# Optimization experiments

Hardware: AMD Instinct MI355X
Metric: run time of the kernel (lower is better)

Reference implementation:

```python
import jax, jax.numpy as jnp
import numpy as np

D_MODEL = 1024
N_HEADS = 16
N_KV = 4
HEAD_DIM = 64
R = 256
B, N = 2, 2048


def setup_inputs() -> dict:
    key = jax.random.key(0)
    ks = jax.random.split(key, 5)
    x = jax.random.normal(ks[0], (B, N, D_MODEL), jnp.float32)
    # rotary cos/sin table: (N, HEAD_DIM//2, 2)
    inv = 1.0 / (10000.0 ** (jnp.arange(0, HEAD_DIM, 2, dtype=jnp.float32) / HEAD_DIM))
    ang = jnp.arange(N, dtype=jnp.float32)[:, None] * inv[None, :]
    freqs_cis = jnp.stack([jnp.cos(ang), jnp.sin(ang)], axis=-1)
    s = 0.02
    Wq = jax.random.normal(ks[1], (D_MODEL, N_HEADS * HEAD_DIM), jnp.float32) * s
    Wk = jax.random.normal(ks[2], (D_MODEL, N_KV * HEAD_DIM), jnp.float32) * s
    Wv = jax.random.normal(ks[3], (D_MODEL, N_KV * HEAD_DIM), jnp.float32) * s
    Wo = jax.random.normal(ks[4], (N_HEADS * HEAD_DIM, D_MODEL), jnp.float32) * s
    return dict(x=x, freqs_cis=freqs_cis, Wq=Wq, Wk=Wk, Wv=Wv, Wo=Wo)


def _select_pairs(scores_i, best_b_i, r):
    """Greedy top-r pair selection with unique-b constraint (one batch row)."""
    half = scores_i.shape[0]
    order = jnp.argsort(-scores_i)  # descending by best similarity

    def step(carry, a_local):
        used, count = carry
        b_local = best_b_i[a_local]
        take = jnp.logical_and(jnp.logical_not(used[b_local]), count < r)
        used = used.at[b_local].set(used[b_local] | take)
        count = count + take.astype(jnp.int32)
        return (used, count), (take, a_local.astype(jnp.int32), b_local.astype(jnp.int32))

    (_, count), (takes, a_locs, b_locs) = jax.lax.scan(
        step, (jnp.zeros(half, bool), jnp.int32(0)), order)
    pos = jnp.cumsum(takes.astype(jnp.int32)) - 1
    idx = jnp.where(takes, pos, r)  # dump non-taken into slot r
    sel_a = jnp.zeros(r + 1, jnp.int32).at[idx].set(a_locs)[:r]
    sel_b = jnp.zeros(r + 1, jnp.int32).at[idx].set(b_locs)[:r]
    valid = jnp.arange(r) < count  # pad (if fewer than r unique) with first pair
    sel_a = jnp.where(valid, sel_a, sel_a[0])
    sel_b = jnp.where(valid, sel_b, sel_b[0])
    return sel_a, sel_b


def bipartite_indices(metric, r):
    """Returns (global_a, global_b, keep_idx) for merge/unmerge."""
    Bm, Nm, _ = metric.shape
    a = metric[:, 0::2]  # (B, half, C)
    b = metric[:, 1::2]
    an = a / jnp.maximum(jnp.linalg.norm(a, axis=-1, keepdims=True), 1e-12)
    bn = b / jnp.maximum(jnp.linalg.norm(b, axis=-1, keepdims=True), 1e-12)
    scores = jnp.einsum('bic,bjc->bij', an, bn)  # (B, half, half)
    best_scores = scores.max(axis=2)
    best_b = scores.argmax(axis=2)
    sel_a, sel_b = jax.vmap(lambda s, m: _select_pairs(s, m, r))(best_scores, best_b)
    global_a = 2 * sel_a      # even indices
    global_b = 2 * sel_b + 1  # odd indices
    bidx = jnp.arange(Bm)[:, None]
    keep_mask = jnp.ones((Bm, Nm), bool).at[bidx, global_b].set(False)
    # stable argsort puts kept (False) positions first, in original order
    keep_idx = jnp.argsort(~keep_mask, axis=1)[:, :Nm - r]
    return global_a, global_b, keep_idx


def merge(x, global_a, global_b, keep_idx):
    Bm = x.shape[0]
    bidx = jnp.arange(Bm)[:, None]
    xa = jnp.take_along_axis(x, global_a[..., None], axis=1)
    xb = jnp.take_along_axis(x, global_b[..., None], axis=1)
    x_out = x.at[bidx, global_a].set((xa + xb) * 0.5)
    return jnp.take_along_axis(x_out, keep_idx[..., None], axis=1)


def unmerge(xm, global_a, global_b, keep_idx, n_orig):
    Bm, _, C = xm.shape
    bidx = jnp.arange(Bm)[:, None]
    out = jnp.zeros((Bm, n_orig, C), xm.dtype).at[bidx, keep_idx].set(xm)
    xa = jnp.take_along_axis(out, global_a[..., None], axis=1)
    return out.at[bidx, global_b].set(xa)


def _rope(t, freqs):
    # t: (B, N, H, HD), freqs: (N, HD//2, 2)
    cos = freqs[None, :, None, :, 0]
    sin = freqs[None, :, None, :, 1]
    t1 = t[..., 0::2]
    t2 = t[..., 1::2]
    rot = jnp.stack([t1 * cos - t2 * sin, t1 * sin + t2 * cos], axis=-1)
    return rot.reshape(t.shape)


def _attention(x_m, freqs, Wq, Wk, Wv, Wo):
    Bm, Nm, _ = x_m.shape
    q = (x_m @ Wq).reshape(Bm, Nm, N_HEADS, HEAD_DIM)
    k = (x_m @ Wk).reshape(Bm, Nm, N_KV, HEAD_DIM)
    v = (x_m @ Wv).reshape(Bm, Nm, N_KV, HEAD_DIM)
    q = _rope(q, freqs)
    k = _rope(k, freqs)
    rep = N_HEADS // N_KV
    k = jnp.repeat(k, rep, axis=2)
    v = jnp.repeat(v, rep, axis=2)
    att = jnp.einsum('bqhd,bkhd->bhqk', q, k) / np.sqrt(HEAD_DIM).astype(np.float32)
    w = jax.nn.softmax(att, axis=-1)
    o = jnp.einsum('bhqk,bkhd->bqhd', w, v).reshape(Bm, Nm, N_HEADS * HEAD_DIM)
    return o @ Wo


def reference(x, freqs_cis, Wq, Wk, Wv, Wo):
    n = x.shape[1]
    metric = jax.lax.stop_gradient(x @ Wk)  # k_proj under no_grad
    ga, gb, ki = bipartite_indices(metric, R)
    x_m = merge(x, ga, gb, ki)
    n_merged = x_m.shape[1]
    out_m = _attention(x_m, freqs_cis[:n_merged], Wq, Wk, Wv, Wo)
    return unmerge(out_m, ga, gb, ki, n)
```

## Files before the change

### kernel.cpp

```cpp
#include <hip/hip_runtime.h>
#include <hip/hip_bf16.h>
#include <math.h>

#define BB 2
#define NN 2048
#define DM 1024
#define NH 16
#define NKV 4
#define HD 64
#define RR 256
#define HALF 1024
#define NM 1792
#define NT 28
#define NSPL 4

typedef __bf16 bf16x8 __attribute__((ext_vector_type(8)));
typedef float f32x4 __attribute__((ext_vector_type(4)));

__device__ inline unsigned pk2(float a, float b) {
  union { __bf16 h; unsigned short u; } ua, ub;
  ua.h = (__bf16)a;
  ub.h = (__bf16)b;
  return (unsigned)ua.u | ((unsigned)ub.u << 16);
}

__device__ inline unsigned shu(unsigned v, int s) {
  return (unsigned)__shfl((int)v, s, 64);
}

__device__ __forceinline__ void async16(const void* g, void* l) {
  __builtin_amdgcn_global_load_lds(
      (const __attribute__((address_space(1))) void*)g,
      (__attribute__((address_space(3))) void*)l, 16, 0, 0);
}

__global__ __launch_bounds__(256) void gemm_bf16(
    const __bf16* __restrict__ A, const __bf16* __restrict__ Bt,
    float* __restrict__ C, int M, int N, int K) {
  __shared__ __align__(16) __bf16 As[8192];
  __shared__ __align__(16) __bf16 Bs[4096];
  const int bm0 = blockIdx.x * 128;
  const int bn0 = blockIdx.y * 64;
  const int w = threadIdx.x >> 6;
  const int lane = threadIdx.x & 63;
  f32x4 acc[2][4];
#pragma unroll
  for (int i = 0; i < 2; ++i)
#pragma unroll
    for (int nt = 0; nt < 4; ++nt) acc[i][nt] = (f32x4){0.f, 0.f, 0.f, 0.f};
  for (int kk = 0; kk < K; kk += 64) {
    __syncthreads();
#pragma unroll
    for (int it = 0; it < 4; ++it) {
      const int c = it * 256 + w * 64 + lane;
      async16(A + (size_t)(bm0 + ((c >> 7) << 4) + (c & 15)) * K + kk +
                  (((c >> 6) & 1) << 5) + (((c >> 4) & 3) << 3),
              &As[(it * 256 + w * 64) * 8]);
    }
#pragma unroll
    for (int it = 0; it < 2; ++it) {
      const int c = it * 256 + w * 64 + lane;
      async16(Bt + (size_t)(bn0 + ((c >> 7) << 4) + (c & 15)) * K + kk +
                  (((c >> 6) & 1) << 5) + (((c >> 4) & 3) << 3),
              &Bs[(it * 256 + w * 64) * 8]);
    }
    __syncthreads();
#pragma unroll
    for (int s = 0; s < 2; ++s) {
      bf16x8 a0 = *(const bf16x8*)&As[((2 * w) * 128 + s * 64 + lane) * 8];
      bf16x8 a1 = *(const bf16x8*)&As[((2 * w + 1) * 128 + s * 64 + lane) * 8];
#pragma unroll
      for (int nt = 0; nt < 4; ++nt) {
        bf16x8 bfr = *(const bf16x8*)&Bs[(nt * 128 + s * 64 + lane) * 8];
        acc[0][nt] =
            __builtin_amdgcn_mfma_f32_16x16x32_bf16(a0, bfr, acc[0][nt], 0, 0, 0);
        acc[1][nt] =
            __builtin_amdgcn_mfma_f32_16x16x32_bf16(a1, bfr, acc[1][nt], 0, 0, 0);
      }
    }
  }
  const int g = lane >> 4, ml = lane & 15;
#pragma unroll
  for (int i = 0; i < 2; ++i)
#pragma unroll
    for (int nt = 0; nt < 4; ++nt)
#pragma unroll
      for (int r = 0; r < 4; ++r)
        C[(size_t)(bm0 + (2 * w + i) * 16 + g * 4 + r) * N + bn0 + nt * 16 +
          ml] = acc[i][nt][r];
}

__global__ __launch_bounds__(256) void gemm_wo(
    const __bf16* __restrict__ A, const __bf16* __restrict__ Bt,
    const int* __restrict__ keep_idx, const int* __restrict__ dst2,
    float* __restrict__ out, int M, int N, int K) {
  __shared__ __align__(16) __bf16 As[8192];
  __shared__ __align__(16) __bf16 Bs[4096];
  const int bm0 = blockIdx.x * 128;
  const int bn0 = blockIdx.y * 64;
  const int w = threadIdx.x >> 6;
  const int lane = threadIdx.x & 63;
  f32x4 acc[2][4];
#pragma unroll
  for (int i = 0; i < 2; ++i)
#pragma unroll
    for (int nt = 0; nt < 4; ++nt) acc[i][nt] = (f32x4){0.f, 0.f, 0.f, 0.f};
  for (int kk = 0; kk < K; kk += 64) {
    __syncthreads();
#pragma unroll
    for (int it = 0; it < 4; ++it) {
      const int c = it * 256 + w * 64 + lane;
      async16(A + (size_t)(bm0 + ((c >> 7) << 4) + (c & 15)) * K + kk +
                  (((c >> 6) & 1) << 5) + (((c >> 4) & 3) << 3),
              &As[(it * 256 + w * 64) * 8]);
    }
#pragma unroll
    for (int it = 0; it < 2; ++it) {
      const int c = it * 256 + w * 64 + lane;
      async16(Bt + (size_t)(bn0 + ((c >> 7) << 4) + (c & 15)) * K + kk +
                  (((c >> 6) & 1) << 5) + (((c >> 4) & 3) << 3),
              &Bs[(it * 256 + w * 64) * 8]);
    }
    __syncthreads();
#pragma unroll
    for (int s = 0; s < 2; ++s) {
      bf16x8 a0 = *(const bf16x8*)&As[((2 * w) * 128 + s * 64 + lane) * 8];
      bf16x8 a1 = *(const bf16x8*)&As[((2 * w + 1) * 128 + s * 64 + lane) * 8];
#pragma unroll
      for (int nt = 0; nt < 4; ++nt) {
        bf16x8 bfr = *(const bf16x8*)&Bs[(nt * 128 + s * 64 + lane) * 8];
        acc[0][nt] =
            __builtin_amdgcn_mfma_f32_16x16x32_bf16(a0, bfr, acc[0][nt], 0, 0, 0);
        acc[1][nt] =
            __builtin_amdgcn_mfma_f32_16x16x32_bf16(a1, bfr, acc[1][nt], 0, 0, 0);
      }
    }
  }
  const int g = lane >> 4, ml = lane & 15;
#pragma unroll
  for (int i = 0; i < 2; ++i)
#pragma unroll
    for (int r = 0; r < 4; ++r) {
      const int row = bm0 + (2 * w + i) * 16 + g * 4 + r;
      const int bb = row / NM, tt = row % NM;
      const int p1 = keep_idx[bb * NM + tt];
      const int p2 = dst2[bb * NM + tt];
#pragma unroll
      for (int nt = 0; nt < 4; ++nt) {
        const int col = bn0 + nt * 16 + ml;
        float v = acc[i][nt][r];
        out[((size_t)(bb * NN + p1)) * DM + col] = v;
        if (p2 >= 0) out[((size_t)(bb * NN + p2)) * DM + col] = v;
      }
    }
}

__global__ __launch_bounds__(256) void gemm3t(
    const __bf16* __restrict__ Ah, const __bf16* __restrict__ Al,
    const __bf16* __restrict__ Bh, const __bf16* __restrict__ Bl,
    float* __restrict__ C0, float* __restrict__ C1, int M, int N, int K) {
  __shared__ __align__(16) __bf16 Ahs[4096], Als[4096], Bhs[4096], Bls[4096];
  const int z = blockIdx.z;
  float* C = z ? C1 : C0;
  const int kof = z * (K / 2);
  const int bm0 = blockIdx.x * 64;
  const int bn0 = blockIdx.y * 64;
  const int w = threadIdx.x >> 6;
  const int lane = threadIdx.x & 63;
  f32x4 acc[4];
#pragma unroll
  for (int nt = 0; nt < 4; ++nt) acc[nt] = (f32x4){0.f, 0.f, 0.f, 0.f};
  for (int kk = kof; kk < kof + K / 2; kk += 64) {
    __syncthreads();
#pragma unroll
    for (int it = 0; it < 2; ++it) {
      const int c = it * 256 + w * 64 + lane;
      const size_t ra = (size_t)(bm0 + ((c >> 7) << 4) + (c & 15)) * K;
      const size_t rb = (size_t)(bn0 + ((c >> 7) << 4) + (c & 15)) * K;
      const int col = kk + (((c >> 6) & 1) << 5) + (((c >> 4) & 3) << 3);
      const int lb = (it * 256 + w * 64) * 8;
      async16(Ah + ra + col, &Ahs[lb]);
      async16(Al + ra + col, &Als[lb]);
      async16(Bh + rb + col, &Bhs[lb]);
      async16(Bl + rb + col, &Bls[lb]);
    }
    __syncthreads();
#pragma unroll
    for (int s = 0; s < 2; ++s) {
      bf16x8 ah = *(const bf16x8*)&Ahs[((w * 2 + s) * 64 + lane) * 8];
      bf16x8 al = *(const bf16x8*)&Als[((w * 2 + s) * 64 + lane) * 8];
#pragma unroll
      for (int nt = 0; nt < 4; ++nt) {
        bf16x8 bh = *(const bf16x8*)&Bhs[((nt * 2 + s) * 64 + lane) * 8];
        bf16x8 bl = *(const bf16x8*)&Bls[((nt * 2 + s) * 64 + lane) * 8];
        acc[nt] = __builtin_amdgcn_mfma_f32_16x16x32_bf16(al, bh, acc[nt], 0, 0, 0);
        acc[nt] = __builtin_amdgcn_mfma_f32_16x16x32_bf16(ah, bl, acc[nt], 0, 0, 0);
        acc[nt] = __builtin_amdgcn_mfma_f32_16x16x32_bf16(ah, bh, acc[nt], 0, 0, 0);
      }
    }
  }
  const int g = lane >> 4, ml = lane & 15;
#pragma unroll
  for (int nt = 0; nt < 4; ++nt)
#pragma unroll
    for (int r = 0; r < 4; ++r)
      C[(size_t)(bm0 + w * 16 + g * 4 + r) * N + bn0 + nt * 16 + ml] =
          acc[nt][r];
}

__global__ __launch_bounds__(256) void gemm_scam(
    const __bf16* __restrict__ Ah, const __bf16* __restrict__ Al,
    const __bf16* __restrict__ Bh, const __bf16* __restrict__ Bl,
    float* __restrict__ sval, int* __restrict__ sidx) {
  __shared__ __align__(16) __bf16 Ahs[4096], Als[4096], Bhs[4096], Bls[4096];
  const size_t zo = (size_t)blockIdx.z * HALF * 256;
  const int bm0 = blockIdx.x * 64;
  const int bn0 = blockIdx.y * 64;
  const int w = threadIdx.x >> 6;
  const int lane = threadIdx.x & 63;
  f32x4 acc[4];
#pragma unroll
  for (int nt = 0; nt < 4; ++nt) acc[nt] = (f32x4){0.f, 0.f, 0.f, 0.f};
  for (int kk = 0; kk < 256; kk += 64) {
    __syncthreads();
#pragma unroll
    for (int it = 0; it < 2; ++it) {
      const int c = it * 256 + w * 64 + lane;
      const size_t ra = zo + (size_t)(bm0 + ((c >> 7) << 4) + (c & 15)) * 256;
      const size_t rb = zo + (size_t)(bn0 + ((c >> 7) << 4) + (c & 15)) * 256;
      const int col = kk + (((c >> 6) & 1) << 5) + (((c >> 4) & 3) << 3);
      const int lb = (it * 256 + w * 64) * 8;
      async16(Ah + ra + col, &Ahs[lb]);
      async16(Al + ra + col, &Als[lb]);
      async16(Bh + rb + col, &Bhs[lb]);
      async16(Bl + rb + col, &Bls[lb]);
    }
    __syncthreads();
#pragma unroll
    for (int s = 0; s < 2; ++s) {
      bf16x8 ah = *(const bf16x8*)&Ahs[((w * 2 + s) * 64 + lane) * 8];
      bf16x8 al = *(const bf16x8*)&Als[((w * 2 + s) * 64 + lane) * 8];
#pragma unroll
      for (int nt = 0; nt < 4; ++nt) {
        bf16x8 bh = *(const bf16x8*)&Bhs[((nt * 2 + s) * 64 + lane) * 8];
        bf16x8 bl = *(const bf16x8*)&Bls[((nt * 2 + s) * 64 + lane) * 8];
        acc[nt] = __builtin_amdgcn_mfma_f32_16x16x32_bf16(al, bh, acc[nt], 0, 0, 0);
        acc[nt] = __builtin_amdgcn_mfma_f32_16x16x32_bf16(ah, bl, acc[nt], 0, 0, 0);
        acc[nt] = __builtin_amdgcn_mfma_f32_16x16x32_bf16(ah, bh, acc[nt], 0, 0, 0);
      }
    }
  }
  const int g = lane >> 4, ml = lane & 15;
#pragma unroll
  for (int r = 0; r < 4; ++r) {
    float bv = acc[0][r];
    int bc = bn0 + ml;
#pragma unroll
    for (int nt = 1; nt < 4; ++nt) {
      float v = acc[nt][r];
      int c = bn0 + nt * 16 + ml;
      if (v > bv) { bv = v; bc = c; }
    }
#pragma unroll
    for (int off = 1; off < 16; off <<= 1) {
      float vo = __shfl_xor(bv, off, 64);
      int co = __shfl_xor(bc, off, 64);
      if (vo > bv || (vo == bv && co < bc)) { bv = vo; bc = co; }
    }
    if (ml == 0) {
      const int row = bm0 + w * 16 + g * 4 + r;
      const size_t o = ((size_t)blockIdx.z * HALF + row) * 16 + (bn0 >> 6);
      sval[o] = bv;
      sidx[o] = bc;
    }
  }
}

__global__ __launch_bounds__(256) void argmax_reduce(
    const float* __restrict__ sval, const int* __restrict__ sidx,
    float* __restrict__ best_s, int* __restrict__ best_b) {
  const int lane = threadIdx.x & 63;
  const int e = lane & 15;
  const int rid = blockIdx.x * 16 + (threadIdx.x >> 6) * 4 + (lane >> 4);
  float bv = sval[rid * 16 + e];
  int bc = sidx[rid * 16 + e];
#pragma unroll
  for (int off = 1; off < 16; off <<= 1) {
    float vo = __shfl_xor(bv, off, 64);
    int co = __shfl_xor(bc, off, 64);
    if (vo > bv || (vo == bv && co < bc)) { bv = vo; bc = co; }
  }
  if (e == 0) {
    best_s[rid] = bv;
    best_b[rid] = bc;
  }
}

__global__ __launch_bounds__(256) void hilo_split(const float* __restrict__ x,
                                                  __bf16* __restrict__ xh,
                                                  __bf16* __restrict__ xl) {
  const int i = blockIdx.x * 256 + threadIdx.x;
  float4 v = ((const float4*)x)[i];
  float f[4] = {v.x, v.y, v.z, v.w};
  union { __bf16 h[4]; uint2 u; } H, L;
#pragma unroll
  for (int j = 0; j < 4; ++j) {
    __bf16 hh = (__bf16)f[j];
    H.h[j] = hh;
    L.h[j] = (__bf16)(f[j] - (float)hh);
  }
  ((uint2*)xh)[i] = H.u;
  ((uint2*)xl)[i] = L.u;
}

__global__ __launch_bounds__(256) void transpose_all(
    const float* __restrict__ Wq, const float* __restrict__ Wk,
    const float* __restrict__ Wv, const float* __restrict__ Wo,
    __bf16* __restrict__ Wqkvt, __bf16* __restrict__ Wktl,
    __bf16* __restrict__ Wot) {
  __shared__ float ld[64][65];
  const int z = blockIdx.x;
  const float* src;
  __bf16* dsth;
  __bf16* dstl = nullptr;
  int N, k0, n0, rowoff;
  if (z < 256) {
    src = Wq; N = 1024; k0 = (z >> 4) << 6; n0 = (z & 15) << 6;
    dsth = Wqkvt; rowoff = 0;
  } else if (z < 320) {
    int zz = z - 256;
    src = Wk; N = 256; k0 = (zz >> 2) << 6; n0 = (zz & 3) << 6;
    dsth = Wqkvt; rowoff = 1024; dstl = Wktl;
  } else if (z < 384) {
    int zz = z - 320;
    src = Wv; N = 256; k0 = (zz >> 2) << 6; n0 = (zz & 3) << 6;
    dsth = Wqkvt; rowoff = 1280;
  } else {
    int zz = z - 384;
    src = Wo; N = 1024; k0 = (zz >> 4) << 6; n0 = (zz & 15) << 6;
    dsth = Wot; rowoff = 0;
  }
  for (int i = threadIdx.x; i < 1024; i += 256) {
    int r = i >> 4, c4 = i & 15;
    float4 v = *(const float4*)(src + (size_t)(k0 + r) * N + n0 + c4 * 4);
    ld[r][c4 * 4 + 0] = v.x;
    ld[r][c4 * 4 + 1] = v.y;
    ld[r][c4 * 4 + 2] = v.z;
    ld[r][c4 * 4 + 3] = v.w;
  }
  __syncthreads();
  for (int i = threadIdx.x; i < 4096; i += 256) {
    int n = i >> 6, k = i & 63;
    float v = ld[k][n];
    __bf16 hh = (__bf16)v;
    dsth[(size_t)(rowoff + n0 + n) * 1024 + k0 + k] = hh;
    if (dstl)
      dstl[(size_t)(n0 + n) * 1024 + k0 + k] = (__bf16)(v - (float)hh);
  }
}

__global__ __launch_bounds__(256) void normalize_split(
    const float* __restrict__ m0, const float* __restrict__ m1,
    __bf16* __restrict__ anh, __bf16* __restrict__ anl,
    __bf16* __restrict__ bnh, __bf16* __restrict__ bnl) {
  const int row = blockIdx.x;
  const int b = row >> 11;
  const int r = row & 2047;
  const int t = threadIdx.x;
  float v = m0[(size_t)row * 256 + t] + m1[(size_t)row * 256 + t];
  float ss = v * v;
#pragma unroll
  for (int o = 32; o > 0; o >>= 1) ss += __shfl_xor(ss, o, 64);
  __shared__ float wsum[4];
  if ((t & 63) == 0) wsum[t >> 6] = ss;
  __syncthreads();
  float tot = wsum[0] + wsum[1] + wsum[2] + wsum[3];
  float inv = 1.f / fmaxf(sqrtf(tot), 1e-12f);
  float nv = v * inv;
  __bf16 hh = (__bf16)nv;
  __bf16 ll = (__bf16)(nv - (float)hh);
  size_t o = ((size_t)b * HALF + (r >> 1)) * 256 + t;
  if (r & 1) {
    bnh[o] = hh;
    bnl[o] = ll;
  } else {
    anh[o] = hh;
    anl[o] = ll;
  }
}

__global__ __launch_bounds__(512) void sort_desc(const float* __restrict__ best_s,
                                                 int* __restrict__ order) {
  const int b = blockIdx.x;
  __shared__ float sv[1024];
  __shared__ int si[1024];
  for (int i = threadIdx.x; i < 1024; i += 512) {
    sv[i] = best_s[b * HALF + i];
    si[i] = i;
  }
  __syncthreads();
  for (int k = 2; k <= 1024; k <<= 1) {
    for (int j = k >> 1; j > 0; j >>= 1) {
      for (int t = threadIdx.x; t < 1024; t += 512) {
        int ixj = t ^ j;
        if (ixj > t) {
          bool dir = ((t & k) == 0);
          float va = sv[t], vb = sv[ixj];
          int ia = si[t], ib = si[ixj];
          bool before = (vb > va) || (vb == va && ib < ia);
          if (before == dir) {
            sv[t] = vb; sv[ixj] = va;
            si[t] = ib; si[ixj] = ia;
          }
        }
      }
      __syncthreads();
    }
  }
  for (int i = threadIdx.x; i < 1024; i += 512) order[b * HALF + i] = si[i];
}

__global__ __launch_bounds__(256) void select_and_index(
    const int* __restrict__ best_b, const int* __restrict__ order,
    int* __restrict__ keep_idx, int* __restrict__ partner,
    int* __restrict__ dst2) {
  const int b = blockIdx.x;
  __shared__ int rankA[HALF];
  __shared__ int minrank[HALF];
  __shared__ int taken[HALF];
  __shared__ int sel_a[RR], sel_b[RR];
  __shared__ int removed[NN];
  __shared__ int src_row[NN];
  __shared__ int tsum[256];
  const int t = threadIdx.x;

  for (int i = t; i < HALF; i += 256) { minrank[i] = 0x7fffffff; taken[i] = 0; }
  for (int i = t; i < NN; i += 256) {
    removed[i] = 0;
    partner[b * NN + i] = -1;
  }
  for (int i = t; i < NM; i += 256) dst2[b * NM + i] = -1;
  __syncthreads();
  int ord[4];
#pragma unroll
  for (int q = 0; q < 4; ++q) {
    int step = t * 4 + q;
    ord[q] = order[b * HALF + step];
    rankA[ord[q]] = step;
  }
  __syncthreads();
#pragma unroll
  for (int q = 0; q < 4; ++q) {
    int a = t * 4 + q;
    atomicMin(&minrank[best_b[b * HALF + a]], rankA[a]);
  }
  __syncthreads();
  for (int i = t; i < HALF; i += 256) {
    int mr = minrank[i];
    if (mr != 0x7fffffff) taken[mr] = 1;
  }
  __syncthreads();
  int c[4];
  int mysum = 0;
#pragma unroll
  for (int q = 0; q < 4; ++q) { c[q] = taken[t * 4 + q]; mysum += c[q]; }
  tsum[t] = mysum;
  __syncthreads();
  for (int off = 1; off < 256; off <<= 1) {
    int v = (t >= off) ? tsum[t - off] : 0;
    __syncthreads();
    tsum[t] += v;
    __syncthreads();
  }
  int run = tsum[t] - mysum;
#pragma unroll
  for (int q = 0; q < 4; ++q) {
    if (c[q] && run < RR) {
      int a = ord[q];
      sel_a[run] = 2 * a;
      sel_b[run] = 2 * best_b[b * HALF + a] + 1;
    }
    run += c[q];
  }
  __syncthreads();
  const int cnt = min(tsum[255], RR);
  if (t >= cnt) { sel_a[t] = sel_a[0]; sel_b[t] = sel_b[0]; }
  __syncthreads();
  {
    int ga = sel_a[t], gb = sel_b[t];
    removed[gb] = 1;
    partner[b * NN + ga] = gb;
  }
  __syncthreads();
  int myc = 0;
#pragma unroll
  for (int q = 0; q < 8; ++q) myc += !removed[8 * t + q];
  tsum[t] = myc;
  __syncthreads();
  for (int off = 1; off < 256; off <<= 1) {
    int v = (t >= off) ? tsum[t - off] : 0;
    __syncthreads();
    tsum[t] += v;
    __syncthreads();
  }
  int pos = tsum[t] - myc;
#pragma unroll
  for (int q = 0; q < 8; ++q) {
    int p = 8 * t + q;
    int sr = -1;
    if (!removed[p]) {
      if (pos < NM) {
        keep_idx[b * NM + pos] = p;
        sr = pos;
      }
      ++pos;
    }
    src_row[p] = sr;
  }
  __syncthreads();
  {
    int sr = src_row[sel_a[t]];
    dst2[b * NM + sr] = sel_b[t];
  }
}

__global__ __launch_bounds__(256) void merge_kernel(
    const float* __restrict__ x, const int* __restrict__ keep_idx,
    const int* __restrict__ partner, __bf16* __restrict__ x_mb) {
  const int mrow = blockIdx.x;
  const int b = mrow / NM;
  const int t = mrow % NM;
  const int p = keep_idx[b * NM + t];
  const int pp = partner[b * NN + p];
  const float4* src =
      reinterpret_cast<const float4*>(x + ((size_t)b * NN + p) * DM);
  float4 val = src[threadIdx.x];
  if (pp >= 0) {
    const float4* s2 =
        reinterpret_cast<const float4*>(x + ((size_t)b * NN + pp) * DM);
    float4 v2 = s2[threadIdx.x];
    val.x = 0.5f * (val.x + v2.x);
    val.y = 0.5f * (val.y + v2.y);
    val.z = 0.5f * (val.z + v2.z);
    val.w = 0.5f * (val.w + v2.w);
  }
  union { __bf16 h[4]; uint2 u; } U;
  U.h[0] = (__bf16)val.x;
  U.h[1] = (__bf16)val.y;
  U.h[2] = (__bf16)val.z;
  U.h[3] = (__bf16)val.w;
  ((uint2*)(x_mb + (size_t)mrow * DM))[threadIdx.x] = U.u;
}

__global__ __launch_bounds__(256) void rope_fused(
    const float* __restrict__ qkv, const float* __restrict__ fc,
    __bf16* __restrict__ qbh, __bf16* __restrict__ kbh) {
  const int row = blockIdx.x;
  const int t = row % NM;
  const int b = row / NM;
  for (int idx = threadIdx.x; idx < 640; idx += 256) {
    int u = idx & 31;
    float c = fc[(t * 32 + u) * 2];
    float s = fc[(t * 32 + u) * 2 + 1];
    if (idx < 512) {
      int h = idx >> 5;
      const float* p = qkv + (size_t)row * 1536 + h * 64 + 2 * u;
      float x1 = p[0], x2 = p[1];
      __bf16* d = qbh + ((size_t)(b * NH + h) * NM + t) * 64 + 2 * u;
      d[0] = (__bf16)((x1 * c - x2 * s) * 0.125f);
      d[1] = (__bf16)((x1 * s + x2 * c) * 0.125f);
    } else {
      int h = (idx - 512) >> 5;
      const float* p = qkv + (size_t)row * 1536 + 1024 + h * 64 + 2 * u;
      float x1 = p[0], x2 = p[1];
      __bf16* d = kbh + ((size_t)(b * NKV + h) * NM + t) * 64 + 2 * u;
      d[0] = (__bf16)(x1 * c - x2 * s);
      d[1] = (__bf16)(x1 * s + x2 * c);
    }
  }
}

__global__ __launch_bounds__(256) void v_repack(const float* __restrict__ qkv,
                                                __bf16* __restrict__ vtb) {
  __shared__ float ld[64][65];
  int bid = blockIdx.x;
  const int kt = bid % (NM / 64); bid /= (NM / 64);
  const int kvh = bid % NKV;
  const int b = bid / NKV;
  const int j0 = kt * 64;
  for (int t2 = threadIdx.x; t2 < 1024; t2 += 256) {
    int key = t2 >> 4, c4 = t2 & 15;
    float4 v4 = *reinterpret_cast<const float4*>(
        qkv + (size_t)(b * NM + j0 + key) * 1536 + 1280 + kvh * 64 + c4 * 4);
    ld[key][c4 * 4 + 0] = v4.x;
    ld[key][c4 * 4 + 1] = v4.y;
    ld[key][c4 * 4 + 2] = v4.z;
    ld[key][c4 * 4 + 3] = v4.w;
  }
  __syncthreads();
  const int dim = threadIdx.x >> 2, kc = threadIdx.x & 3;
  __bf16* out = vtb + ((size_t)(b * NKV + kvh) * 64 + dim) * NM + j0 + kc * 16;
#pragma unroll
  for (int kk = 0; kk < 16; ++kk) out[kk] = (__bf16)ld[kc * 16 + kk][dim];
}

__global__ __launch_bounds__(512) void attn_mfma(
    const __bf16* __restrict__ qbh, const __bf16* __restrict__ kbh,
    const __bf16* __restrict__ vtb, float* __restrict__ pl,
    __bf16* __restrict__ pacc) {
  __shared__ __align__(16) __bf16 Ks[4096];
  __shared__ __align__(16) __bf16 Vs[4096];
  int bid = blockIdx.x;
  const int qt2 = bid % (NM / 32); bid /= (NM / 32);
  const int split = bid % NSPL; bid /= NSPL;
  const int kvh = bid % NKV;
  const int b = bid / NKV;
  const int w = threadIdx.x >> 6;
  const int lane = threadIdx.x & 63;
  const int h = kvh * 4 + (w & 3);
  const int qt = qt2 * 32 + (w >> 2) * 16;
  const int g = lane >> 4;
  const int ml = lane & 15;

  const __bf16* qrow = qbh + ((size_t)(b * NH + h) * NM + qt + ml) * 64;
  bf16x8 qa0 = *reinterpret_cast<const bf16x8*>(qrow + g * 8);
  bf16x8 qa1 = *reinterpret_cast<const bf16x8*>(qrow + 32 + g * 8);

  f32x4 acc[4];
#pragma unroll
  for (int mt = 0; mt < 4; ++mt) acc[mt] = (f32x4){0.f, 0.f, 0.f, 0.f};
  float lsum = 0.f;

  const __bf16* kp = kbh + (size_t)(b * NKV + kvh) * NM * 64;
  const __bf16* vp = vtb + (size_t)(b * NKV + kvh) * 64 * NM;
  const int src0 = ((lane >> 4) & 1) * 32 + ml;
  const int src1 = src0 + 16;
  const int sel = g >> 1;

  const int jt0 = split * (NT / NSPL);
  for (int jt = jt0; jt < jt0 + NT / NSPL; ++jt) {
    __syncthreads();
    {
      const int c = threadIdx.x;
      const int lb = (w * 64) * 8;
      async16(kp + (size_t)(jt * 64 + ((c >> 7) << 4) + (c & 15)) * 64 +
                  (((c >> 6) & 1) << 5) + (((c >> 4) & 3) << 3),
              &Ks[lb]);
      async16(vp + (size_t)(((c >> 7) << 4) + (c & 15)) * NM + jt * 64 +
                  (((c >> 6) & 1) << 5) + (((c >> 4) & 3) << 3),
              &Vs[lb]);
    }
    __syncthreads();
    f32x4 S[4];
#pragma unroll
    for (int nt = 0; nt < 4; ++nt) {
      bf16x8 k0 = *(const bf16x8*)&Ks[(nt * 128 + lane) * 8];
      bf16x8 k1 = *(const bf16x8*)&Ks[(nt * 128 + 64 + lane) * 8];
      f32x4 s4 = (f32x4){0.f, 0.f, 0.f, 0.f};
      s4 = __builtin_amdgcn_mfma_f32_16x16x32_bf16(k0, qa0, s4, 0, 0, 0);
      s4 = __builtin_amdgcn_mfma_f32_16x16x32_bf16(k1, qa1, s4, 0, 0, 0);
      S[nt] = s4;
    }
    float p[4][4];
#pragma unroll
    for (int nt = 0; nt < 4; ++nt)
#pragma unroll
      for (int r = 0; r < 4; ++r) {
        p[nt][r] = __expf(S[nt][r]);
        lsum += p[nt][r];
      }
    unsigned pk[4][2];
#pragma unroll
    for (int nt = 0; nt < 4; ++nt) {
      pk[nt][0] = pk2(p[nt][0], p[nt][1]);
      pk[nt][1] = pk2(p[nt][2], p[nt][3]);
    }
    unsigned A00 = shu(pk[0][0], src0), A01 = shu(pk[0][1], src0);
    unsigned A10 = shu(pk[1][0], src0), A11 = shu(pk[1][1], src0);
    unsigned B00 = shu(pk[0][0], src1), B01 = shu(pk[0][1], src1);
    unsigned B10 = shu(pk[1][0], src1), B11 = shu(pk[1][1], src1);
    unsigned C00 = shu(pk[2][0], src0), C01 = shu(pk[2][1], src0);
    unsigned C10 = shu(pk[3][0], src0), C11 = shu(pk[3][1], src0);
    unsigned D00 = shu(pk[2][0], src1), D01 = shu(pk[2][1], src1);
    unsigned D10 = shu(pk[3][0], src1), D11 = shu(pk[3][1], src1);
    union { uint4 u; bf16x8 v; } P0, P1;
    P0.u.x = sel ? A10 : A00; P0.u.y = sel ? A11 : A01;
    P0.u.z = sel ? B10 : B00; P0.u.w = sel ? B11 : B01;
    P1.u.x = sel ? C10 : C00; P1.u.y = sel ? C11 : C01;
    P1.u.z = sel ? D10 : D00; P1.u.w = sel ? D11 : D01;
#pragma unroll
    for (int mt = 0; mt < 4; ++mt) {
      bf16x8 v0 = *(const bf16x8*)&Vs[(mt * 128 + lane) * 8];
      bf16x8 v1 = *(const bf16x8*)&Vs[(mt * 128 + 64 + lane) * 8];
      acc[mt] = __builtin_amdgcn_mfma_f32_16x16x32_bf16(v0, P0.v, acc[mt], 0, 0, 0);
      acc[mt] = __builtin_amdgcn_mfma_f32_16x16x32_bf16(v1, P1.v, acc[mt], 0, 0, 0);
    }
  }
  lsum += __shfl_xor(lsum, 16, 64);
  lsum += __shfl_xor(lsum, 32, 64);
  const size_t row = (size_t)(b * NH + h) * NM + qt + ml;
  if (g == 0) pl[row * NSPL + split] = lsum;
  __bf16* pa = pacc + (row * NSPL + split) * 64;
#pragma unroll
  for (int mt = 0; mt < 4; ++mt) {
    uint2 u;
    u.x = pk2(acc[mt][0], acc[mt][1]);
    u.y = pk2(acc[mt][2], acc[mt][3]);
    *reinterpret_cast<uint2*>(pa + mt * 16 + g * 4) = u;
  }
}

__global__ __launch_bounds__(256) void attn_combine(
    const float* __restrict__ pl, const __bf16* __restrict__ pacc,
    __bf16* __restrict__ attn_ob) {
  const size_t rid = (size_t)blockIdx.x * 4 + (threadIdx.x >> 6);
  const int d = threadIdx.x & 63;
  float num = 0.f, den = 0.f;
#pragma unroll
  for (int s = 0; s < NSPL; ++s) {
    num += (float)pacc[(rid * NSPL + s) * 64 + d];
    den += pl[rid * NSPL + s];
  }
  float o = num / den;
  const int q = (int)(rid % NM);
  const int h = (int)((rid / NM) % NH);
  const int b = (int)(rid / ((size_t)NM * NH));
  attn_ob[((size_t)(b * NM + q)) * DM + h * 64 + d] = (__bf16)o;
}

extern "C" void kernel_launch(void* const* d_in, const int* in_sizes, int n_in,
                              void* d_out, int out_size, void* d_ws,
                              size_t ws_size, hipStream_t stream) {
  const float* x = (const float*)d_in[0];
  const float* fc = (const float*)d_in[1];
  const float* Wq = (const float*)d_in[2];
  const float* Wk = (const float*)d_in[3];
  const float* Wv = (const float*)d_in[4];
  const float* Wo = (const float*)d_in[5];
  float* out = (float*)d_out;

  char* ws = (char*)d_ws;
  size_t off = 0;
  auto alloc = [&](size_t bytes) {
    void* p = ws + off;
    off += (bytes + 255) & ~(size_t)255;
    return p;
  };
  float* metric0 = (float*)alloc((size_t)BB * NN * 256 * 4);
  float* metric1 = (float*)alloc((size_t)BB * NN * 256 * 4);
  float* best_s = (float*)alloc((size_t)BB * HALF * 4);
  int* best_b = (int*)alloc((size_t)BB * HALF * 4);
  int* order = (int*)alloc((size_t)BB * HALF * 4);
  int* keep_idx = (int*)alloc((size_t)BB * NM * 4);
  int* partner = (int*)alloc((size_t)BB * NN * 4);
  int* dst2 = (int*)alloc((size_t)BB * NM * 4);
  float* sval = (float*)alloc((size_t)BB * HALF * 16 * 4);
  int* sidx = (int*)alloc((size_t)BB * HALF * 16 * 4);
  char* bigreg = (char*)alloc((size_t)30 * 1024 * 1024);
  __bf16* xh = (__bf16*)bigreg;
  __bf16* xl = (__bf16*)(bigreg + (size_t)8704 * 1024);
  __bf16* anh = (__bf16*)bigreg;
  __bf16* anl = (__bf16*)(bigreg + (size_t)1100 * 1024);
  __bf16* bnh = (__bf16*)(bigreg + (size_t)2200 * 1024);
  __bf16* bnl = (__bf16*)(bigreg + (size_t)3300 * 1024);
  float* qkv = (float*)bigreg;
  __bf16* pacc = (__bf16*)bigreg;
  __bf16* x_mb = (__bf16*)alloc((size_t)BB * NM * DM * 2);
  __bf16* qbh = (__bf16*)alloc((size_t)BB * NH * NM * 64 * 2);
  __bf16* kbh = (__bf16*)alloc((size_t)BB * NKV * NM * 64 * 2);
  __bf16* vtb = (__bf16*)alloc((size_t)BB * NKV * 64 * NM * 2);
  __bf16* attn_ob = (__bf16*)alloc((size_t)BB * NM * DM * 2);
  float* pl = (float*)alloc((size_t)BB * NH * NM * NSPL * 4);
  __bf16* Wqkvt = (__bf16*)alloc((size_t)1536 * DM * 2);
  __bf16* Wktl = (__bf16*)alloc((size_t)256 * DM * 2);
  __bf16* Wot = (__bf16*)alloc((size_t)DM * DM * 2);
  const __bf16* Wkth = Wqkvt + (size_t)1024 * 1024;

  transpose_all<<<640, 256, 0, stream>>>(Wq, Wk, Wv, Wo, Wqkvt, Wktl, Wot);
  hilo_split<<<(BB * NN * DM / 4) / 256, 256, 0, stream>>>(x, xh, xl);
  gemm3t<<<dim3(64, 4, 2), 256, 0, stream>>>(xh, xl, Wkth, Wktl, metric0,
                                             metric1, BB * NN, 256, DM);
  normalize_split<<<BB * NN, 256, 0, stream>>>(metric0, metric1, anh, anl, bnh,
                                               bnl);
  gemm_scam<<<dim3(16, 16, 2), 256, 0, stream>>>(anh, anl, bnh, bnl, sval,
                                                 sidx);
  argmax_reduce<<<(BB * HALF) / 16, 256, 0, stream>>>(sval, sidx, best_s,
                                                      best_b);
  sort_desc<<<BB, 512, 0, stream>>>(best_s, order);
  select_and_index<<<BB, 256, 0, stream>>>(best_b, order, keep_idx, partner,
                                           dst2);
  merge_kernel<<<BB * NM, 256, 0, stream>>>(x, keep_idx, partner, x_mb);
  gemm_bf16<<<dim3(28, 24), 256, 0, stream>>>(x_mb, Wqkvt, qkv, BB * NM, 1536,
                                              DM);
  rope_fused<<<BB * NM, 256, 0, stream>>>(qkv, fc, qbh, kbh);
  v_repack<<<BB * NKV * (NM / 64), 256, 0, stream>>>(qkv, vtb);
  attn_mfma<<<BB * NKV * NSPL * (NM / 32), 512, 0, stream>>>(qbh, kbh, vtb, pl,
                                                             pacc);
  attn_combine<<<(BB * NH * NM) / 4, 256, 0, stream>>>(pl, pacc, attn_ob);
  gemm_wo<<<dim3(28, 16), 256, 0, stream>>>(attn_ob, Wot, keep_idx, dst2, out,
                                            BB * NM, DM, DM);
}
```

Measured before the change: 283.6 us.

## Merge small prep kernels, fold argmax into sort, double-buffer attention K/V loads

After: 291.6 us. 1.03x slower.

```diff
diff --git a/kernel.cpp b/kernel.cpp
--- a/kernel.cpp
+++ b/kernel.cpp
@@ -276,50 +276,29 @@
   }
 }
 
-__global__ __launch_bounds__(256) void argmax_reduce(
-    const float* __restrict__ sval, const int* __restrict__ sidx,
-    float* __restrict__ best_s, int* __restrict__ best_b) {
-  const int lane = threadIdx.x & 63;
-  const int e = lane & 15;
-  const int rid = blockIdx.x * 16 + (threadIdx.x >> 6) * 4 + (lane >> 4);
-  float bv = sval[rid * 16 + e];
-  int bc = sidx[rid * 16 + e];
-#pragma unroll
-  for (int off = 1; off < 16; off <<= 1) {
-    float vo = __shfl_xor(bv, off, 64);
-    int co = __shfl_xor(bc, off, 64);
-    if (vo > bv || (vo == bv && co < bc)) { bv = vo; bc = co; }
-  }
-  if (e == 0) {
-    best_s[rid] = bv;
-    best_b[rid] = bc;
-  }
-}
-
-__global__ __launch_bounds__(256) void hilo_split(const float* __restrict__ x,
-                                                  __bf16* __restrict__ xh,
-                                                  __bf16* __restrict__ xl) {
-  const int i = blockIdx.x * 256 + threadIdx.x;
-  float4 v = ((const float4*)x)[i];
-  float f[4] = {v.x, v.y, v.z, v.w};
-  union { __bf16 h[4]; uint2 u; } H, L;
-#pragma unroll
-  for (int j = 0; j < 4; ++j) {
-    __bf16 hh = (__bf16)f[j];
-    H.h[j] = hh;
-    L.h[j] = (__bf16)(f[j] - (float)hh);
-  }
-  ((uint2*)xh)[i] = H.u;
-  ((uint2*)xl)[i] = L.u;
-}
-
-__global__ __launch_bounds__(256) void transpose_all(
+__global__ __launch_bounds__(256) void prep_in(
     const float* __restrict__ Wq, const float* __restrict__ Wk,
     const float* __restrict__ Wv, const float* __restrict__ Wo,
-    __bf16* __restrict__ Wqkvt, __bf16* __restrict__ Wktl,
-    __bf16* __restrict__ Wot) {
+    const float* __restrict__ x, __bf16* __restrict__ Wqkvt,
+    __bf16* __restrict__ Wktl, __bf16* __restrict__ Wot,
+    __bf16* __restrict__ xh, __bf16* __restrict__ xl) {
+  const int z = blockIdx.x;
+  if (z >= 640) {
+    const int i = (z - 640) * 256 + threadIdx.x;
+    float4 v = ((const float4*)x)[i];
+    float f[4] = {v.x, v.y, v.z, v.w};
+    union { __bf16 h[4]; uint2 u; } H, L;
+#pragma unroll
+    for (int j = 0; j < 4; ++j) {
+      __bf16 hh = (__bf16)f[j];
+      H.h[j] = hh;
+      L.h[j] = (__bf16)(f[j] - (float)hh);
+    }
+    ((uint2*)xh)[i] = H.u;
+    ((uint2*)xl)[i] = L.u;
+    return;
+  }
   __shared__ float ld[64][65];
-  const int z = blockIdx.x;
   const float* src;
   __bf16* dsth;
   __bf16* dstl = nullptr;
@@ -389,14 +368,25 @@
   }
 }
 
-__global__ __launch_bounds__(512) void sort_desc(const float* __restrict__ best_s,
-                                                 int* __restrict__ order) {
+__global__ __launch_bounds__(512) void sort_desc(
+    const float* __restrict__ sval, const int* __restrict__ sidx,
+    int* __restrict__ best_b, int* __restrict__ order) {
   const int b = blockIdx.x;
   __shared__ float sv[1024];
   __shared__ int si[1024];
   for (int i = threadIdx.x; i < 1024; i += 512) {
-    sv[i] = best_s[b * HALF + i];
+    const size_t base = ((size_t)b * HALF + i) * 16;
+    float bv = sval[base];
+    int bc = sidx[base];
+#pragma unroll
+    for (int e = 1; e < 16; ++e) {
+      float v = sval[base + e];
+      int c = sidx[base + e];
+      if (v > bv || (v == bv && c < bc)) { bv = v; bc = c; }
+    }
+    sv[i] = bv;
     si[i] = i;
+    best_b[b * HALF + i] = bc;
   }
   __syncthreads();
   for (int k = 2; k <= 1024; k <<= 1) {
@@ -552,38 +542,39 @@
   ((uint2*)(x_mb + (size_t)mrow * DM))[threadIdx.x] = U.u;
 }
 
-__global__ __launch_bounds__(256) void rope_fused(
+__global__ __launch_bounds__(256) void prep_qkv(
     const float* __restrict__ qkv, const float* __restrict__ fc,
-    __bf16* __restrict__ qbh, __bf16* __restrict__ kbh) {
-  const int row = blockIdx.x;
-  const int t = row % NM;
-  const int b = row / NM;
-  for (int idx = threadIdx.x; idx < 640; idx += 256) {
-    int u = idx & 31;
-    float c = fc[(t * 32 + u) * 2];
-    float s = fc[(t * 32 + u) * 2 + 1];
-    if (idx < 512) {
-      int h = idx >> 5;
-      const float* p = qkv + (size_t)row * 1536 + h * 64 + 2 * u;
-      float x1 = p[0], x2 = p[1];
-      __bf16* d = qbh + ((size_t)(b * NH + h) * NM + t) * 64 + 2 * u;
-      d[0] = (__bf16)((x1 * c - x2 * s) * 0.125f);
-      d[1] = (__bf16)((x1 * s + x2 * c) * 0.125f);
-    } else {
-      int h = (idx - 512) >> 5;
-      const float* p = qkv + (size_t)row * 1536 + 1024 + h * 64 + 2 * u;
-      float x1 = p[0], x2 = p[1];
-      __bf16* d = kbh + ((size_t)(b * NKV + h) * NM + t) * 64 + 2 * u;
-      d[0] = (__bf16)(x1 * c - x2 * s);
-      d[1] = (__bf16)(x1 * s + x2 * c);
-    }
-  }
-}
-
-__global__ __launch_bounds__(256) void v_repack(const float* __restrict__ qkv,
-                                                __bf16* __restrict__ vtb) {
+    __bf16* __restrict__ qbh, __bf16* __restrict__ kbh,
+    __bf16* __restrict__ vtb) {
   __shared__ float ld[64][65];
-  int bid = blockIdx.x;
+  const int z = blockIdx.x;
+  if (z < BB * NM) {
+    const int row = z;
+    const int t = row % NM;
+    const int b = row / NM;
+    for (int idx = threadIdx.x; idx < 640; idx += 256) {
+      int u = idx & 31;
+      float c = fc[(t * 32 + u) * 2];
+      float s = fc[(t * 32 + u) * 2 + 1];
+      if (idx < 512) {
+        int h = idx >> 5;
+        const float* p = qkv + (size_t)row * 1536 + h * 64 + 2 * u;
+        float x1 = p[0], x2 = p[1];
+        __bf16* d = qbh + ((size_t)(b * NH + h) * NM + t) * 64 + 2 * u;
+        d[0] = (__bf16)((x1 * c - x2 * s) * 0.125f);
+        d[1] = (__bf16)((x1 * s + x2 * c) * 0.125f);
+      } else {
+        int h = (idx - 512) >> 5;
+        const float* p = qkv + (size_t)row * 1536 + 1024 + h * 64 + 2 * u;
+        float x1 = p[0], x2 = p[1];
+        __bf16* d = kbh + ((size_t)(b * NKV + h) * NM + t) * 64 + 2 * u;
+        d[0] = (__bf16)(x1 * c - x2 * s);
+        d[1] = (__bf16)(x1 * s + x2 * c);
+      }
+    }
+    return;
+  }
+  int bid = z - BB * NM;
   const int kt = bid % (NM / 64); bid /= (NM / 64);
   const int kvh = bid % NKV;
   const int b = bid / NKV;
@@ -608,8 +599,8 @@
     const __bf16* __restrict__ qbh, const __bf16* __restrict__ kbh,
     const __bf16* __restrict__ vtb, float* __restrict__ pl,
     __bf16* __restrict__ pacc) {
-  __shared__ __align__(16) __bf16 Ks[4096];
-  __shared__ __align__(16) __bf16 Vs[4096];
+  __shared__ __align__(16) __bf16 Ks[2][4096];
+  __shared__ __align__(16) __bf16 Vs[2][4096];
   int bid = blockIdx.x;
   const int qt2 = bid % (NM / 32); bid /= (NM / 32);
   const int split = bid % NSPL; bid /= NSPL;
@@ -636,26 +627,32 @@
   const int src0 = ((lane >> 4) & 1) * 32 + ml;
   const int src1 = src0 + 16;
   const int sel = g >> 1;
+  const int c = threadIdx.x;
+  const int lb = w * 512;
+  const size_t koff = (size_t)(((c >> 7) << 4) + (c & 15)) * 64 +
+                      (((c >> 6) & 1) << 5) + (((c >> 4) & 3) << 3);
+  const size_t voff = (size_t)(((c >> 7) << 4) + (c & 15)) * NM +
+                      (((c >> 6) & 1) << 5) + (((c >> 4) & 3) << 3);
 
   const int jt0 = split * (NT / NSPL);
-  for (int jt = jt0; jt < jt0 + NT / NSPL; ++jt) {
-    __syncthreads();
-    {
-      const int c = threadIdx.x;
-      const int lb = (w * 64) * 8;
-      async16(kp + (size_t)(jt * 64 + ((c >> 7) << 4) + (c & 15)) * 64 +
-                  (((c >> 6) & 1) << 5) + (((c >> 4) & 3) << 3),
-              &Ks[lb]);
-      async16(vp + (size_t)(((c >> 7) << 4) + (c & 15)) * NM + jt * 64 +
-                  (((c >> 6) & 1) << 5) + (((c >> 4) & 3) << 3),
-              &Vs[lb]);
-    }
-    __syncthreads();
+  const int niter = NT / NSPL;
+  async16(kp + (size_t)jt0 * 64 * 64 + koff, &Ks[0][lb]);
+  async16(vp + jt0 * 64 + voff, &Vs[0][lb]);
+
+  for (int i = 0; i < niter; ++i) {
+    __syncthreads();
+    if (i + 1 < niter) {
+      const int jn = jt0 + i + 1;
+      async16(kp + (size_t)jn * 64 * 64 + koff, &Ks[(i + 1) & 1][lb]);
+      async16(vp + jn * 64 + voff, &Vs[(i + 1) & 1][lb]);
+    }
+    const __bf16* Kb = Ks[i & 1];
+    const __bf16* Vb = Vs[i & 1];
     f32x4 S[4];
 #pragma unroll
     for (int nt = 0; nt < 4; ++nt) {
-      bf16x8 k0 = *(const bf16x8*)&Ks[(nt * 128 + lane) * 8];
-      bf16x8 k1 = *(const bf16x8*)&Ks[(nt * 128 + 64 + lane) * 8];
+      bf16x8 k0 = *(const bf16x8*)&Kb[(nt * 128 + lane) * 8];
+      bf16x8 k1 = *(const bf16x8*)&Kb[(nt * 128 + 64 + lane) * 8];
       f32x4 s4 = (f32x4){0.f, 0.f, 0.f, 0.f};
       s4 = __builtin_amdgcn_mfma_f32_16x16x32_bf16(k0, qa0, s4, 0, 0, 0);
       s4 = __builtin_amdgcn_mfma_f32_16x16x32_bf16(k1, qa1, s4, 0, 0, 0);
@@ -690,8 +687,8 @@
     P1.u.z = sel ? D10 : D00; P1.u.w = sel ? D11 : D01;
 #pragma unroll
     for (int mt = 0; mt < 4; ++mt) {
-      bf16x8 v0 = *(const bf16x8*)&Vs[(mt * 128 + lane) * 8];
-      bf16x8 v1 = *(const bf16x8*)&Vs[(mt * 128 + 64 + lane) * 8];
+      bf16x8 v0 = *(const bf16x8*)&Vb[(mt * 128 + lane) * 8];
+      bf16x8 v1 = *(const bf16x8*)&Vb[(mt * 128 + 64 + lane) * 8];
       acc[mt] = __builtin_amdgcn_mfma_f32_16x16x32_bf16(v0, P0.v, acc[mt], 0, 0, 0);
       acc[mt] = __builtin_amdgcn_mfma_f32_16x16x32_bf16(v1, P1.v, acc[mt], 0, 0, 0);
     }
@@ -748,7 +745,6 @@
   };
   float* metric0 = (float*)alloc((size_t)BB * NN * 256 * 4);
   float* metric1 = (float*)alloc((size_t)BB * NN * 256 * 4);
-  float* best_s = (float*)alloc((size_t)BB * HALF * 4);
   int* best_b = (int*)alloc((size_t)BB * HALF * 4);
   int* order = (int*)alloc((size_t)BB * HALF * 4);
   int* keep_idx = (int*)alloc((size_t)BB * NM * 4);
@@ -776,24 +772,22 @@
   __bf16* Wot = (__bf16*)alloc((size_t)DM * DM * 2);
   const __bf16* Wkth = Wqkvt + (size_t)1024 * 1024;
 
-  transpose_all<<<640, 256, 0, stream>>>(Wq, Wk, Wv, Wo, Wqkvt, Wktl, Wot);
-  hilo_split<<<(BB * NN * DM / 4) / 256, 256, 0, stream>>>(x, xh, xl);
+  prep_in<<<640 + (BB * NN * DM / 4) / 256, 256, 0, stream>>>(
+      Wq, Wk, Wv, Wo, x, Wqkvt, Wktl, Wot, xh, xl);
   gemm3t<<<dim3(64, 4, 2), 256, 0, stream>>>(xh, xl, Wkth, Wktl, metric0,
                                              metric1, BB * NN, 256, DM);
   normalize_split<<<BB * NN, 256, 0, stream>>>(metric0, metric1, anh, anl, bnh,
                                                bnl);
   gemm_scam<<<dim3(16, 16, 2), 256, 0, stream>>>(anh, anl, bnh, bnl, sval,
                                                  sidx);
-  argmax_reduce<<<(BB * HALF) / 16, 256, 0, stream>>>(sval, sidx, best_s,
-                                                      best_b);
-  sort_desc<<<BB, 512, 0, stream>>>(best_s, order);
+  sort_desc<<<BB, 512, 0, stream>>>(sval, sidx, best_b, order);
   select_and_index<<<BB, 256, 0, stream>>>(best_b, order, keep_idx, partner,
                                            dst2);
   merge_kernel<<<BB * NM, 256, 0, stream>>>(x, keep_idx, partner, x_mb);
   gemm_bf16<<<dim3(28, 24), 256, 0, stream>>>(x_mb, Wqkvt, qkv, BB * NM, 1536,
                                               DM);
-  rope_fused<<<BB * NM, 256, 0, stream>>>(qkv, fc, qbh, kbh);
-  v_repack<<<BB * NKV * (NM / 64), 256, 0, stream>>>(qkv, vtb);
+  prep_qkv<<<BB * NM + BB * NKV * (NM / 64), 256, 0, stream>>>(qkv, fc, qbh,
+                                                               kbh, vtb);
   attn_mfma<<<BB * NKV * NSPL * (NM / 32), 512, 0, stream>>>(qbh, kbh, vtb, pl,
                                                              pacc);
   attn_combine<<<(BB * NH * NM) / 4, 256, 0, stream>>>(pl, pacc, attn_ob);
```
